# Optimization experiments

Hardware: AMD Instinct MI355X
Metric: run time of the kernel (lower is better)

The kernel has to match this reference:

```python
import jax, jax.numpy as jnp
import numpy as np

N = 30000      # nodes
E = 480000     # edges (avg degree 16)
IN = 128       # input_size
HID = 128      # hidden_size
H = 4          # heads
C = HID // H   # channels per head = 32
NEG_SLOPE = 0.2


def gat_layer(x, src, dst, W, al, ar, act):
    """DGL-style GATConv: x (N, Fin) -> (N, h*c). al, ar: (h, c)."""
    n = x.shape[0]
    h, c = al.shape
    f = (x @ W).reshape(n, h, c)                      # projected features
    el = jnp.sum(f * al, axis=-1)                     # (N, h)
    er = jnp.sum(f * ar, axis=-1)                     # (N, h)
    e = jax.nn.leaky_relu(el[src] + er[dst], NEG_SLOPE)  # (E, h) edge scores
    # edge softmax over incoming edges of each dst node
    m = jax.lax.stop_gradient(jax.ops.segment_max(e, dst, num_segments=n))
    a = jnp.exp(e - m[dst])
    z = jax.ops.segment_sum(a, dst, num_segments=n)   # (N, h)
    alpha = a / z[dst]                                # (E, h)
    out = jax.ops.segment_sum(alpha[:, :, None] * f[src], dst, num_segments=n)
    out = out.reshape(n, h * c)
    return act(out) if act is not None else out


def setup_inputs() -> dict:
    key = jax.random.key(0)
    ks = jax.random.split(key, 14)
    s = 0.1
    return {
        "inputs": jax.random.normal(ks[0], (N, IN), jnp.float32),
        "src": jax.random.randint(ks[1], (E,), 0, N, dtype=jnp.int32),
        "dst": jax.random.randint(ks[2], (E,), 0, N, dtype=jnp.int32),
        "W0": jax.random.normal(ks[3], (IN, H * C), jnp.float32) * s,
        "al0": jax.random.normal(ks[4], (H, C), jnp.float32) * s,
        "ar0": jax.random.normal(ks[5], (H, C), jnp.float32) * s,
        "W1": jax.random.normal(ks[6], (H * C, H * C), jnp.float32) * s,
        "al1": jax.random.normal(ks[7], (H, C), jnp.float32) * s,
        "ar1": jax.random.normal(ks[8], (H, C), jnp.float32) * s,
        "W2": jax.random.normal(ks[9], (H * C, H * HID), jnp.float32) * s,
        "al2": jax.random.normal(ks[10], (H, HID), jnp.float32) * s,
        "ar2": jax.random.normal(ks[11], (H, HID), jnp.float32) * s,
        "fc_w": jax.random.normal(ks[12], (H * HID, 8), jnp.float32) * s,
        "fc_b": jnp.zeros((8,), jnp.float32),
    }


def reference(inputs, src, dst, W0, al0, ar0, W1, al1, ar1, W2, al2, ar2, fc_w, fc_b):
    h = gat_layer(inputs, src, dst, W0, al0, ar0, jax.nn.relu)
    h = gat_layer(h, src, dst, W1, al1, ar1, jax.nn.relu)
    h = gat_layer(h, src, dst, W2, al2, ar2, None)      # (N, H*HID)
    h = jax.nn.relu(h)                                  # dropout p=0 is identity
    pooled = jnp.max(h, axis=0, keepdims=True)          # global max pooling -> (1, H*HID)
    logits = pooled @ fc_w + fc_b                       # (1, 8)
    return jax.nn.softmax(logits, axis=-1)
```

## Files before the change

### kernel.cpp

```cpp
#include <hip/hip_runtime.h>

#define HH 4

typedef __attribute__((ext_vector_type(8))) short bf16x8;
typedef __attribute__((ext_vector_type(4))) float f32x4;

__device__ __forceinline__ float lrelu(float v) { return (v >= 0.0f) ? v : 0.2f * v; }

__device__ __forceinline__ unsigned short f2bf(float x) {
    union { float f; unsigned u; } v; v.f = x;
    unsigned r = (v.u + 0x7FFFu + ((v.u >> 16) & 1u)) >> 16;
    return (unsigned short)r;
}
__device__ __forceinline__ float bf2f(unsigned short b) {
    union { unsigned u; float f; } v; v.u = ((unsigned)b) << 16;
    return v.f;
}
__device__ __forceinline__ float bf2f_lo(unsigned u) {
    union { unsigned x; float f; } v; v.x = u << 16;
    return v.f;
}
__device__ __forceinline__ float bf2f_hi(unsigned u) {
    union { unsigned x; float f; } v; v.x = u & 0xffff0000u;
    return v.f;
}

__global__ void hist_kernel(const int* __restrict__ dst, int* __restrict__ deg, int E) {
    int i = blockIdx.x * blockDim.x + threadIdx.x;
    if (i < E) atomicAdd(&deg[dst[i]], 1);
}

__global__ void scan_block(const int* __restrict__ deg, int* __restrict__ rs,
                           int* __restrict__ bsum, int n) {
    __shared__ int buf[1024];
    int i = blockIdx.x * 1024 + threadIdx.x;
    int v = (i < n) ? deg[i] : 0;
    buf[threadIdx.x] = v;
    __syncthreads();
    for (int off = 1; off < 1024; off <<= 1) {
        int t = (threadIdx.x >= off) ? buf[threadIdx.x - off] : 0;
        __syncthreads();
        buf[threadIdx.x] += t;
        __syncthreads();
    }
    if (i < n) rs[i + 1] = buf[threadIdx.x];
    if (threadIdx.x == 1023) bsum[blockIdx.x] = buf[1023];
}

__global__ void scan_top(int* bsum, int nb) {
    if (threadIdx.x == 0 && blockIdx.x == 0) {
        int acc = 0;
        for (int b = 0; b < nb; ++b) { int t = bsum[b]; bsum[b] = acc; acc += t; }
    }
}

__global__ void scan_add(int* __restrict__ rs, const int* __restrict__ bsum, int n) {
    int i = blockIdx.x * blockDim.x + threadIdx.x;
    if (i == 0) rs[0] = 0;
    if (i < n) rs[i + 1] += bsum[i >> 10];
}

__global__ void scatter_kernel(const int* __restrict__ src, const int* __restrict__ dst,
                               const int* __restrict__ rs, int* __restrict__ cur,
                               int* __restrict__ csrc, int E) {
    int i = blockIdx.x * blockDim.x + threadIdx.x;
    if (i >= E) return;
    int d = dst[i];
    int p = rs[d] + atomicAdd(&cur[d], 1);
    csrc[p] = src[i];
}

__global__ void prep_all(const float* __restrict__ W0, const float* __restrict__ W1,
                         const float* __restrict__ W2, const float* __restrict__ al2,
                         const float* __restrict__ ar2, bf16x8* __restrict__ WFH,
                         bf16x8* __restrict__ WFL, float* __restrict__ wl,
                         float* __restrict__ wr, int* __restrict__ zerop, int nzero) {
    if (blockIdx.x < 48) {
        const int wid = blockIdx.x * 4 + (threadIdx.x >> 6);
        const int l = threadIdx.x & 63;
        const int lr = l & 15, lg = l >> 4;
        int t = wid;
        const float* srcp;
        int stride, coff;
        if (t < 32) { srcp = W0; stride = 128; coff = 0; }
        else if (t < 64) { srcp = W1; stride = 128; coff = 0; t -= 32; }
        else { t -= 64; srcp = W2; stride = 512; coff = (t >> 5) * 128; t &= 31; }
        const int kt = t >> 3, ct = t & 7;
        bf16x8 h8, l8;
#pragma unroll
        for (int j = 0; j < 8; ++j) {
            float w = srcp[(size_t)(kt * 32 + lg * 8 + j) * stride + coff + ct * 16 + lr];
            unsigned short hb = f2bf(w);
            h8[j] = (short)hb;
            l8[j] = (short)f2bf(w - bf2f(hb));
        }
        WFH[(size_t)wid * 64 + l] = h8;
        WFL[(size_t)wid * 64 + l] = l8;
    } else if (blockIdx.x == 48) {
        int idx = threadIdx.x;
#pragma unroll
        for (int k = 0; k < 2; ++k, idx += 256) {
            int h = idx >> 7, i = idx & 127;
            float sl = 0.0f, sr = 0.0f;
            for (int c = 0; c < 128; ++c) {
                float w = W2[(size_t)i * 512 + h * 128 + c];
                sl = fmaf(w, al2[h * 128 + c], sl);
                sr = fmaf(w, ar2[h * 128 + c], sr);
            }
            wl[idx] = sl;
            wr[idx] = sr;
        }
    } else {
        int idx = (blockIdx.x - 49) * 256 + threadIdx.x;
        if (idx < nzero) zerop[idx] = 0;
    }
}

template <int SPLIT_A>
__global__ __launch_bounds__(256) void mfma_gemm128(const float* __restrict__ xf,
                                                    const unsigned short* __restrict__ xbf,
                                                    const bf16x8* __restrict__ BH,
                                                    const bf16x8* __restrict__ BL,
                                                    unsigned short* __restrict__ fbf,
                                                    const float* __restrict__ al,
                                                    const float* __restrict__ ar,
                                                    float* __restrict__ el,
                                                    float* __restrict__ er, int n) {
    const int tid = threadIdx.x;
    const int w = tid >> 6, l = tid & 63;
    const int lr = l & 15, lg = l >> 4;
    const int rowbase = blockIdx.x * 64 + w * 16;
    const int arow = rowbase + lr;

    f32x4 acc[8];
#pragma unroll
    for (int ct = 0; ct < 8; ++ct) acc[ct] = (f32x4){0.f, 0.f, 0.f, 0.f};

    for (int kt = 0; kt < 4; ++kt) {
        bf16x8 ah, alo;
        if (SPLIT_A) {
            float a[8];
            if (arow < n) {
                float4 p0 = *reinterpret_cast<const float4*>(&xf[(size_t)arow * 128 + kt * 32 + lg * 8]);
                float4 p1 = *reinterpret_cast<const float4*>(&xf[(size_t)arow * 128 + kt * 32 + lg * 8 + 4]);
                a[0] = p0.x; a[1] = p0.y; a[2] = p0.z; a[3] = p0.w;
                a[4] = p1.x; a[5] = p1.y; a[6] = p1.z; a[7] = p1.w;
            } else {
#pragma unroll
                for (int j = 0; j < 8; ++j) a[j] = 0.f;
            }
#pragma unroll
            for (int j = 0; j < 8; ++j) {
                unsigned short hb = f2bf(a[j]);
                ah[j] = (short)hb;
                alo[j] = (short)f2bf(a[j] - bf2f(hb));
            }
        } else {
            ah = (bf16x8){0, 0, 0, 0, 0, 0, 0, 0};
            if (arow < n)
                ah = *reinterpret_cast<const bf16x8*>(&xbf[(size_t)arow * 128 + kt * 32 + lg * 8]);
        }
        const bf16x8* bh = &BH[(size_t)(kt * 8) * 64 + l];
        const bf16x8* bl = &BL[(size_t)(kt * 8) * 64 + l];
#pragma unroll
        for (int ct = 0; ct < 8; ++ct) {
            bf16x8 b1 = bh[ct * 64];
            bf16x8 b2 = bl[ct * 64];
            acc[ct] = __builtin_amdgcn_mfma_f32_16x16x32_bf16(ah, b1, acc[ct], 0, 0, 0);
            if (SPLIT_A)
                acc[ct] = __builtin_amdgcn_mfma_f32_16x16x32_bf16(alo, b1, acc[ct], 0, 0, 0);
            acc[ct] = __builtin_amdgcn_mfma_f32_16x16x32_bf16(ah, b2, acc[ct], 0, 0, 0);
        }
    }
#pragma unroll
    for (int reg = 0; reg < 4; ++reg) {
        int orow = rowbase + lg * 4 + reg;
        if (orow < n) {
#pragma unroll
            for (int ct = 0; ct < 8; ++ct)
                fbf[(size_t)orow * 128 + ct * 16 + lr] = f2bf(acc[ct][reg]);
        }
    }
    float pel[4][4], per_[4][4];
#pragma unroll
    for (int h = 0; h < 4; ++h) {
        float a0 = al[h * 32 + lr], a1 = al[h * 32 + 16 + lr];
        float r0 = ar[h * 32 + lr], r1 = ar[h * 32 + 16 + lr];
#pragma unroll
        for (int reg = 0; reg < 4; ++reg) {
            pel[reg][h] = acc[2 * h][reg] * a0 + acc[2 * h + 1][reg] * a1;
            per_[reg][h] = acc[2 * h][reg] * r0 + acc[2 * h + 1][reg] * r1;
        }
    }
#pragma unroll
    for (int off = 1; off < 16; off <<= 1) {
#pragma unroll
        for (int reg = 0; reg < 4; ++reg)
#pragma unroll
            for (int h = 0; h < 4; ++h) {
                pel[reg][h] += __shfl_xor(pel[reg][h], off);
                per_[reg][h] += __shfl_xor(per_[reg][h], off);
            }
    }
    if (lr == 0) {
#pragma unroll
        for (int reg = 0; reg < 4; ++reg) {
            int orow = rowbase + lg * 4 + reg;
            if (orow < n) {
#pragma unroll
                for (int h = 0; h < 4; ++h) {
                    el[orow * HH + h] = pel[reg][h];
                    er[orow * HH + h] = per_[reg][h];
                }
            }
        }
    }
}

__global__ __launch_bounds__(256) void mfma_bd_pool(const unsigned short* __restrict__ aggbf,
                                                    const bf16x8* __restrict__ WFH,
                                                    const bf16x8* __restrict__ WFL,
                                                    unsigned* __restrict__ pooled, int n) {
    __shared__ float smax[4][128];
    const int tid = threadIdx.x;
    const int w = tid >> 6, l = tid & 63;
    const int lr = l & 15, lg = l >> 4;
    const int y = blockIdx.y;
    const int rowbase = blockIdx.x * 64 + w * 16;
    const int arow = rowbase + lr;
    const bf16x8* BH = WFH + (size_t)(64 + y * 32) * 64;
    const bf16x8* BL = WFL + (size_t)(64 + y * 32) * 64;

    f32x4 acc[8];
#pragma unroll
    for (int ct = 0; ct < 8; ++ct) acc[ct] = (f32x4){0.f, 0.f, 0.f, 0.f};

    for (int kt = 0; kt < 4; ++kt) {
        bf16x8 av = {0, 0, 0, 0, 0, 0, 0, 0};
        if (arow < n)
            av = *reinterpret_cast<const bf16x8*>(&aggbf[(size_t)arow * 512 + y * 128 + kt * 32 + lg * 8]);
        const bf16x8* bh = &BH[(size_t)(kt * 8) * 64 + l];
        const bf16x8* bl = &BL[(size_t)(kt * 8) * 64 + l];
#pragma unroll
        for (int ct = 0; ct < 8; ++ct) {
            acc[ct] = __builtin_amdgcn_mfma_f32_16x16x32_bf16(av, bh[ct * 64], acc[ct], 0, 0, 0);
            acc[ct] = __builtin_amdgcn_mfma_f32_16x16x32_bf16(av, bl[ct * 64], acc[ct], 0, 0, 0);
        }
    }
    float cm[8];
#pragma unroll
    for (int ct = 0; ct < 8; ++ct) {
        float v = fmaxf(fmaxf(acc[ct][0], acc[ct][1]), fmaxf(acc[ct][2], acc[ct][3]));
        cm[ct] = fmaxf(v, 0.f);
    }
#pragma unroll
    for (int ct = 0; ct < 8; ++ct) {
        cm[ct] = fmaxf(cm[ct], __shfl_xor(cm[ct], 16));
        cm[ct] = fmaxf(cm[ct], __shfl_xor(cm[ct], 32));
    }
    if (l < 16) {
#pragma unroll
        for (int ct = 0; ct < 8; ++ct) smax[w][ct * 16 + lr] = cm[ct];
    }
    __syncthreads();
    if (tid < 128) {
        float mx = fmaxf(fmaxf(smax[0][tid], smax[1][tid]), fmaxf(smax[2][tid], smax[3][tid]));
        atomicMax(&pooled[y * 128 + tid], __float_as_uint(mx));
    }
}

template <int MODE>
__global__ __launch_bounds__(256) void aggr_wave128(const int* __restrict__ rs,
                                                    const int* __restrict__ csrc,
                                                    const float* __restrict__ el,
                                                    const float* __restrict__ er,
                                                    const unsigned short* __restrict__ fbf,
                                                    unsigned short* __restrict__ outbf,
                                                    const float* __restrict__ wl,
                                                    const float* __restrict__ wr,
                                                    float* __restrict__ el2,
                                                    float* __restrict__ er2, int n) {
    int d = blockIdx.x * 4 + (threadIdx.x >> 6);
    if (d >= n) return;
    d = __builtin_amdgcn_readfirstlane(d);
    const int lane = threadIdx.x & 63;
    const int hg = lane >> 4;
    const int cb2 = lane * 2;
    const int e0 = __builtin_amdgcn_readfirstlane(rs[d]);
    const int e1 = __builtin_amdgcn_readfirstlane(rs[d + 1]);
    const float erd = er[d * HH + hg];

    float z = 0.f, a0 = 0.f, a1 = 0.f;
#pragma unroll 4
    for (int e = e0; e < e1; ++e) {
        int s = csrc[e];
        float v = el[s * HH + hg] + erd;
        float wv = __expf(lrelu(v));
        z += wv;
        unsigned xu = *reinterpret_cast<const unsigned*>(&fbf[(size_t)s * 128 + cb2]);
        a0 = fmaf(wv, bf2f_lo(xu), a0);
        a1 = fmaf(wv, bf2f_hi(xu), a1);
    }
    const float rz = (z > 0.f) ? 1.0f / z : 0.f;
    a0 = fmaxf(a0 * rz, 0.f);
    a1 = fmaxf(a1 * rz, 0.f);
    ushort2 sv;
    sv.x = f2bf(a0); sv.y = f2bf(a1);
    *reinterpret_cast<ushort2*>(&outbf[(size_t)d * 128 + cb2]) = sv;
    if (MODE == 1) {
        float pl[4], pr[4];
#pragma unroll
        for (int h = 0; h < 4; ++h) {
            float2 wlv = *reinterpret_cast<const float2*>(&wl[h * 128 + cb2]);
            float2 wrv = *reinterpret_cast<const float2*>(&wr[h * 128 + cb2]);
            pl[h] = a0 * wlv.x + a1 * wlv.y;
            pr[h] = a0 * wrv.x + a1 * wrv.y;
        }
#pragma unroll
        for (int off = 1; off < 64; off <<= 1) {
#pragma unroll
            for (int h = 0; h < 4; ++h) {
                pl[h] += __shfl_xor(pl[h], off);
                pr[h] += __shfl_xor(pr[h], off);
            }
        }
        if (lane == 0) {
#pragma unroll
            for (int h = 0; h < 4; ++h) {
                el2[d * HH + h] = pl[h];
                er2[d * HH + h] = pr[h];
            }
        }
    }
}

__global__ __launch_bounds__(256) void aggr_x(const int* __restrict__ rs,
                                              const int* __restrict__ csrc,
                                              const float* __restrict__ el,
                                              const float* __restrict__ er,
                                              const unsigned short* __restrict__ xbf,
                                              unsigned short* __restrict__ aggbf, int n) {
    int d = blockIdx.x * 4 + (threadIdx.x >> 6);
    if (d >= n) return;
    d = __builtin_amdgcn_readfirstlane(d);
    const int lane = threadIdx.x & 63;
    const int hg = lane >> 4, j16 = lane & 15;
    const int e0 = __builtin_amdgcn_readfirstlane(rs[d]);
    const int e1 = __builtin_amdgcn_readfirstlane(rs[d + 1]);
    const float erd = er[d * HH + hg];

    float z = 0.f;
    float acc[8];
#pragma unroll
    for (int j = 0; j < 8; ++j) acc[j] = 0.f;
#pragma unroll 2
    for (int e = e0; e < e1; ++e) {
        int s = csrc[e];
        float v = el[s * HH + hg] + erd;
        float wv = __expf(lrelu(v));
        z += wv;
        uint4 xu = *reinterpret_cast<const uint4*>(&xbf[(size_t)s * 128 + j16 * 8]);
        acc[0] = fmaf(wv, bf2f_lo(xu.x), acc[0]);
        acc[1] = fmaf(wv, bf2f_hi(xu.x), acc[1]);
        acc[2] = fmaf(wv, bf2f_lo(xu.y), acc[2]);
        acc[3] = fmaf(wv, bf2f_hi(xu.y), acc[3]);
        acc[4] = fmaf(wv, bf2f_lo(xu.z), acc[4]);
        acc[5] = fmaf(wv, bf2f_hi(xu.z), acc[5]);
        acc[6] = fmaf(wv, bf2f_lo(xu.w), acc[6]);
        acc[7] = fmaf(wv, bf2f_hi(xu.w), acc[7]);
    }
    const float rz = (z > 0.f) ? 1.0f / z : 0.f;
    ushort4 s0, s1;
    s0.x = f2bf(acc[0] * rz); s0.y = f2bf(acc[1] * rz);
    s0.z = f2bf(acc[2] * rz); s0.w = f2bf(acc[3] * rz);
    s1.x = f2bf(acc[4] * rz); s1.y = f2bf(acc[5] * rz);
    s1.z = f2bf(acc[6] * rz); s1.w = f2bf(acc[7] * rz);
    unsigned short* op = &aggbf[(size_t)d * 512 + hg * 128 + j16 * 8];
    *reinterpret_cast<ushort4*>(op) = s0;
    *reinterpret_cast<ushort4*>(op + 4) = s1;
}

__global__ void head_kernel(const float* __restrict__ pooled, const float* __restrict__ fcw,
                            const float* __restrict__ fcb, float* __restrict__ out) {
    __shared__ float logits[8];
    int t = threadIdx.x;
    if (t < 8) {
        float acc = fcb[t];
        for (int i = 0; i < 512; ++i) acc = fmaf(pooled[i], fcw[i * 8 + t], acc);
        logits[t] = acc;
    }
    __syncthreads();
    if (t == 0) {
        float mx = -1e30f;
        for (int j = 0; j < 8; ++j) mx = fmaxf(mx, logits[j]);
        float ex[8], s = 0.0f;
        for (int j = 0; j < 8; ++j) { ex[j] = expf(logits[j] - mx); s += ex[j]; }
        for (int j = 0; j < 8; ++j) out[j] = ex[j] / s;
    }
}

extern "C" void kernel_launch(void* const* d_in, const int* in_sizes, int n_in,
                              void* d_out, int out_size, void* d_ws, size_t ws_size,
                              hipStream_t stream) {
    const float* x0  = (const float*)d_in[0];
    const int*   src = (const int*)d_in[1];
    const int*   dst = (const int*)d_in[2];
    const float* W0  = (const float*)d_in[3];
    const float* al0 = (const float*)d_in[4];
    const float* ar0 = (const float*)d_in[5];
    const float* W1  = (const float*)d_in[6];
    const float* al1 = (const float*)d_in[7];
    const float* ar1 = (const float*)d_in[8];
    const float* W2  = (const float*)d_in[9];
    const float* al2 = (const float*)d_in[10];
    const float* ar2 = (const float*)d_in[11];
    const float* fcw = (const float*)d_in[12];
    const float* fcb = (const float*)d_in[13];
    float* outp = (float*)d_out;

    const int N = in_sizes[0] / 128;
    const int E = in_sizes[1];

    float* el   = (float*)d_ws;
    float* er   = el + (size_t)N * HH;
    float* el2  = er + (size_t)N * HH;
    float* er2  = el2 + (size_t)N * HH;
    float* wl   = er2 + (size_t)N * HH;
    float* wr   = wl + 512;
    int* deg  = (int*)(wr + 512);
    int* cur  = deg + N;
    float* pooled = (float*)(cur + N);
    int* rs   = (int*)(pooled + 512);
    int* bsum = rs + (N + 1);
    int* csrc = bsum + 64;
    unsigned short* Fbf   = (unsigned short*)(csrc + E);
    unsigned short* B0bf  = Fbf + (size_t)N * 128;
    unsigned short* B1bf  = B0bf + (size_t)N * 128;
    unsigned short* AGGbf = B1bf + (size_t)N * 128;
    uintptr_t wfaddr = ((uintptr_t)(AGGbf + (size_t)N * 512) + 15) & ~(uintptr_t)15;
    bf16x8* WFH = (bf16x8*)wfaddr;
    bf16x8* WFL = WFH + (size_t)192 * 64;

    const int nzero = 2 * N + 512;
    const int zb = (nzero + 255) / 256;
    prep_all<<<49 + zb, 256, 0, stream>>>(W0, W1, W2, al2, ar2, WFH, WFL, wl, wr, deg, nzero);
    hist_kernel<<<(E + 255) / 256, 256, 0, stream>>>(dst, deg, E);
    const int nb = (N + 1023) / 1024;
    scan_block<<<nb, 1024, 0, stream>>>(deg, rs, bsum, N);
    scan_top<<<1, 64, 0, stream>>>(bsum, nb);
    scan_add<<<(N + 255) / 256, 256, 0, stream>>>(rs, bsum, N);
    scatter_kernel<<<(E + 255) / 256, 256, 0, stream>>>(src, dst, rs, cur, csrc, E);

    const int rowTiles = (N + 63) / 64;
    const int nodeBlocks = (N + 3) / 4;

    mfma_gemm128<1><<<rowTiles, 256, 0, stream>>>(x0, nullptr, WFH, WFL, Fbf, al0, ar0, el, er, N);
    aggr_wave128<0><<<nodeBlocks, 256, 0, stream>>>(rs, csrc, el, er, Fbf, B0bf,
                                                    nullptr, nullptr, nullptr, nullptr, N);
    mfma_gemm128<0><<<rowTiles, 256, 0, stream>>>(nullptr, B0bf, WFH + (size_t)32 * 64,
                                                  WFL + (size_t)32 * 64, Fbf, al1, ar1, el, er, N);
    aggr_wave128<1><<<nodeBlocks, 256, 0, stream>>>(rs, csrc, el, er, Fbf, B1bf,
                                                    wl, wr, el2, er2, N);
    aggr_x<<<nodeBlocks, 256, 0, stream>>>(rs, csrc, el2, er2, B1bf, AGGbf, N);
    mfma_bd_pool<<<dim3(rowTiles, 4), 256, 0, stream>>>(AGGbf, WFH, WFL, (unsigned*)pooled, N);

    head_kernel<<<1, 64, 0, stream>>>(pooled, fcw, fcb, outp);
}
```

Baseline: 239.2 us.

## Fold scan_top into scan_add and head into pool kernel via last-block ticket

Drops the single-thread scan_top launch by having each scan_add thread sum the preceding block totals itself. It also removes the separate head_kernel launch: the pooling kernel takes an atomic ticket, and the last block to finish computes the FC layer and softmax. Loop unroll factors in the two aggregation kernels are raised. This cuts two kernel launches and their serialization gaps, at the cost of a threadfence and atomic per block, redundant prefix sums per thread, and a tail of work done serially by one block.

Result: slower. 308.0 us (+28.8%).

```diff
diff --git a/kernel.cpp b/kernel.cpp
--- a/kernel.cpp
+++ b/kernel.cpp
@@ -47,17 +47,15 @@
     if (threadIdx.x == 1023) bsum[blockIdx.x] = buf[1023];
 }
 
-__global__ void scan_top(int* bsum, int nb) {
-    if (threadIdx.x == 0 && blockIdx.x == 0) {
-        int acc = 0;
-        for (int b = 0; b < nb; ++b) { int t = bsum[b]; bsum[b] = acc; acc += t; }
-    }
-}
-
 __global__ void scan_add(int* __restrict__ rs, const int* __restrict__ bsum, int n) {
     int i = blockIdx.x * blockDim.x + threadIdx.x;
     if (i == 0) rs[0] = 0;
-    if (i < n) rs[i + 1] += bsum[i >> 10];
+    if (i < n) {
+        int blk = i >> 10;
+        int pre = 0;
+        for (int b = 0; b < blk; ++b) pre += bsum[b];
+        rs[i + 1] += pre;
+    }
 }
 
 __global__ void scatter_kernel(const int* __restrict__ src, const int* __restrict__ dst,
@@ -220,8 +218,13 @@
 __global__ __launch_bounds__(256) void mfma_bd_pool(const unsigned short* __restrict__ aggbf,
                                                     const bf16x8* __restrict__ WFH,
                                                     const bf16x8* __restrict__ WFL,
-                                                    unsigned* __restrict__ pooled, int n) {
+                                                    unsigned* __restrict__ pooled,
+                                                    int* __restrict__ ticket,
+                                                    const float* __restrict__ fcw,
+                                                    const float* __restrict__ fcb,
+                                                    float* __restrict__ outp, int n) {
     __shared__ float smax[4][128];
+    __shared__ int isLast;
     const int tid = threadIdx.x;
     const int w = tid >> 6, l = tid & 63;
     const int lr = l & 15, lg = l >> 4;
@@ -266,6 +269,32 @@
     if (tid < 128) {
         float mx = fmaxf(fmaxf(smax[0][tid], smax[1][tid]), fmaxf(smax[2][tid], smax[3][tid]));
         atomicMax(&pooled[y * 128 + tid], __float_as_uint(mx));
+    }
+    __syncthreads();
+    if (tid == 0) {
+        __threadfence();
+        int done = atomicAdd(ticket, 1);
+        isLast = (done == (int)(gridDim.x * gridDim.y) - 1);
+    }
+    __syncthreads();
+    if (isLast) {
+        __shared__ float logits[8];
+        if (tid < 8) {
+            float accl = fcb[tid];
+            for (int i = 0; i < 512; ++i) {
+                float pv = __uint_as_float(((volatile unsigned*)pooled)[i]);
+                accl = fmaf(pv, fcw[i * 8 + tid], accl);
+            }
+            logits[tid] = accl;
+        }
+        __syncthreads();
+        if (tid == 0) {
+            float mx = -1e30f;
+            for (int j = 0; j < 8; ++j) mx = fmaxf(mx, logits[j]);
+            float ex[8], s = 0.0f;
+            for (int j = 0; j < 8; ++j) { ex[j] = expf(logits[j] - mx); s += ex[j]; }
+            for (int j = 0; j < 8; ++j) outp[j] = ex[j] / s;
+        }
     }
 }
 
@@ -291,7 +320,7 @@
     const float erd = er[d * HH + hg];
 
     float z = 0.f, a0 = 0.f, a1 = 0.f;
-#pragma unroll 4
+#pragma unroll 8
     for (int e = e0; e < e1; ++e) {
         int s = csrc[e];
         float v = el[s * HH + hg] + erd;
@@ -353,7 +382,7 @@
     float acc[8];
 #pragma unroll
     for (int j = 0; j < 8; ++j) acc[j] = 0.f;
-#pragma unroll 2
+#pragma unroll 4
     for (int e = e0; e < e1; ++e) {
         int s = csrc[e];
         float v = el[s * HH + hg] + erd;
@@ -378,25 +407,6 @@
     unsigned short* op = &aggbf[(size_t)d * 512 + hg * 128 + j16 * 8];
     *reinterpret_cast<ushort4*>(op) = s0;
     *reinterpret_cast<ushort4*>(op + 4) = s1;
-}
-
-__global__ void head_kernel(const float* __restrict__ pooled, const float* __restrict__ fcw,
-                            const float* __restrict__ fcb, float* __restrict__ out) {
-    __shared__ float logits[8];
-    int t = threadIdx.x;
-    if (t < 8) {
-        float acc = fcb[t];
-        for (int i = 0; i < 512; ++i) acc = fmaf(pooled[i], fcw[i * 8 + t], acc);
-        logits[t] = acc;
-    }
-    __syncthreads();
-    if (t == 0) {
-        float mx = -1e30f;
-        for (int j = 0; j < 8; ++j) mx = fmaxf(mx, logits[j]);
-        float ex[8], s = 0.0f;
-        for (int j = 0; j < 8; ++j) { ex[j] = expf(logits[j] - mx); s += ex[j]; }
-        for (int j = 0; j < 8; ++j) out[j] = ex[j] / s;
-    }
 }
 
 extern "C" void kernel_launch(void* const* d_in, const int* in_sizes, int n_in,
@@ -430,7 +440,8 @@
     int* deg  = (int*)(wr + 512);
     int* cur  = deg + N;
     float* pooled = (float*)(cur + N);
-    int* rs   = (int*)(pooled + 512);
+    int* ticket = (int*)(pooled + 512);
+    int* rs   = ticket + 1;
     int* bsum = rs + (N + 1);
     int* csrc = bsum + 64;
     unsigned short* Fbf   = (unsigned short*)(csrc + E);
@@ -441,13 +452,12 @@
     bf16x8* WFH = (bf16x8*)wfaddr;
     bf16x8* WFL = WFH + (size_t)192 * 64;
 
-    const int nzero = 2 * N + 512;
+    const int nzero = 2 * N + 513;
     const int zb = (nzero + 255) / 256;
     prep_all<<<49 + zb, 256, 0, stream>>>(W0, W1, W2, al2, ar2, WFH, WFL, wl, wr, deg, nzero);
     hist_kernel<<<(E + 255) / 256, 256, 0, stream>>>(dst, deg, E);
     const int nb = (N + 1023) / 1024;
     scan_block<<<nb, 1024, 0, stream>>>(deg, rs, bsum, N);
-    scan_top<<<1, 64, 0, stream>>>(bsum, nb);
     scan_add<<<(N + 255) / 256, 256, 0, stream>>>(rs, bsum, N);
     scatter_kernel<<<(E + 255) / 256, 256, 0, stream>>>(src, dst, rs, cur, csrc, E);
 
@@ -462,7 +472,6 @@
     aggr_wave128<1><<<nodeBlocks, 256, 0, stream>>>(rs, csrc, el, er, Fbf, B1bf,
                                                     wl, wr, el2, er2, N);
     aggr_x<<<nodeBlocks, 256, 0, stream>>>(rs, csrc, el2, er2, B1bf, AGGbf, N);
-    mfma_bd_pool<<<dim3(rowTiles, 4), 256, 0, stream>>>(AGGbf, WFH, WFL, (unsigned*)pooled, N);
-
-    head_kernel<<<1, 64, 0, stream>>>(pooled, fcw, fcb, outp);
-}
+    mfma_bd_pool<<<dim3(rowTiles, 4), 256, 0, stream>>>(AGGbf, WFH, WFL, (unsigned*)pooled,
+                                                        ticket, fcw, fcb, outp, N);
+}
```
